# Kernel tuning notes

Hardware: AMD Instinct MI355X
Metric: run time of the kernel (lower is better)

## Reference

```python
import jax, jax.numpy as jnp
import numpy as np
import math

# Static problem sizes (match input_specs)
B, TQ, SQ, TK, SK = 1, 8, 256, 32, 1024
DM, NH = 1024, 8
HD = DM // NH            # 128; mrope_section sums to HD//2
MROPE = [16, 24, 24]
ROPE_BASE = 10000.0


def _build_indices():
    """Reproduce create_idx_cube + slow/fast index selection (all static)."""
    T_max = max(TQ, TK)
    H_max = int(math.sqrt(max(SQ, SK)))
    cube = np.stack(np.meshgrid(np.arange(T_max), np.arange(H_max), np.arange(H_max), indexing='ij'), axis=-1)  # (T,H,W,3)
    # slow (query) indices
    t_idx = np.linspace(0, T_max - 1, TQ).astype(int)
    slow = cube[t_idx]
    if SQ < SK:
        h_q = int(math.sqrt(SQ))
        hi = np.linspace(0, H_max, 2 * h_q + 1).astype(int)[1:-1][::2]
        slow = slow[:, hi][:, :, hi]
    # fast (key) indices
    h_k = int(math.sqrt(SK))
    hf = np.linspace(0, H_max, 2 * h_k + 1).astype(int)[1:-1][::2]
    fast = cube[:, hf][:, :, hf]
    return slow.reshape(-1, 3).T, fast.reshape(-1, 3).T, max(T_max, H_max)


_slow_np, _fast_np, _SEQ = _build_indices()
SLOW_POS = jnp.asarray(_slow_np)   # (3, TQ*SQ) int
FAST_POS = jnp.asarray(_fast_np)   # (3, TK*SK) int

# Standard rotary tables: cos/sin of shape (seq_len, HD)
_inv = 1.0 / (ROPE_BASE ** (np.arange(0, HD, 2, dtype=np.float32) / HD))
_freqs = np.outer(np.arange(_SEQ, dtype=np.float32), _inv)
_emb = np.concatenate([_freqs, _freqs], axis=-1)
COS = jnp.asarray(np.cos(_emb), dtype=jnp.float32)
SIN = jnp.asarray(np.sin(_emb), dtype=jnp.float32)

# per-channel axis (t/h/w) selector, equivalent to the split/concat with i%3
AXIS_MAP = jnp.asarray(np.concatenate([np.full(m, i % 3) for i, m in enumerate(MROPE * 2)]))  # (HD,)


def rotate_half(x):
    return jnp.concatenate([-x[..., HD // 2:], x[..., :HD // 2]], axis=-1)


def apply_mrope(x, pos):
    # x: (B, NH, N, HD); pos: (3, N)
    cos_g = jnp.take_along_axis(COS[pos], AXIS_MAP[None, None, :], axis=0)[0]  # (N, HD)
    sin_g = jnp.take_along_axis(SIN[pos], AXIS_MAP[None, None, :], axis=0)[0]
    return x * cos_g[None, None] + rotate_half(x) * sin_g[None, None]


def setup_inputs() -> dict:
    key = jax.random.key(0)
    ks = jax.random.split(key, 9)
    s = 0.02
    return {
        'q': jax.random.normal(ks[0], (B, TQ, SQ, DM), jnp.float32),
        'k': jax.random.normal(ks[1], (B, TK, SK, DM), jnp.float32),
        'v': jax.random.normal(ks[2], (B, TK, SK, DM), jnp.float32),
        'Wq': jax.random.normal(ks[3], (DM, DM), jnp.float32) * s,
        'bq': jnp.zeros((DM,), jnp.float32),
        'Wk': jax.random.normal(ks[4], (DM, DM), jnp.float32) * s,
        'bk': jnp.zeros((DM,), jnp.float32),
        'Wv': jax.random.normal(ks[5], (DM, DM), jnp.float32) * s,
        'bv': jnp.zeros((DM,), jnp.float32),
    }


def reference(q, k, v, Wq, bq, Wk, bk, Wv, bv):
    # QKV projections -> (B, NH, N, HD)
    qh = (q.reshape(B, TQ * SQ, DM) @ Wq + bq).reshape(B, TQ * SQ, NH, HD).transpose(0, 2, 1, 3)
    kh = (k.reshape(B, TK * SK, DM) @ Wk + bk).reshape(B, TK * SK, NH, HD).transpose(0, 2, 1, 3)
    vh = (v.reshape(B, TK * SK, DM) @ Wv + bv).reshape(B, TK * SK, NH, HD).transpose(0, 2, 1, 3)
    # multimodal 3D RoPE on q (slow frames) and k (fast frames)
    qh = apply_mrope(qh, SLOW_POS)
    kh = apply_mrope(kh, FAST_POS)
    # group time: each query frame attends to its r = TK//TQ aligned kv frames
    r = TK // TQ
    qg = qh.reshape(NH, TQ, SQ, HD).transpose(1, 0, 2, 3)          # (TQ, NH, SQ, HD)
    kg = kh.reshape(NH, TQ, r * SK, HD).transpose(1, 0, 2, 3)      # (TQ, NH, r*SK, HD)
    vg = vh.reshape(NH, TQ, r * SK, HD).transpose(1, 0, 2, 3)
    scores = jnp.einsum('thqd,thkd->thqk', qg, kg) / math.sqrt(HD)
    attn = jax.nn.softmax(scores, axis=-1)
    out = jnp.einsum('thqk,thkd->thqd', attn, vg)                  # (TQ, NH, SQ, HD)
    return out.transpose(0, 2, 1, 3).reshape(B, TQ, SQ, DM)
```

## Files before the change

### kernel.cpp

```cpp
#include <hip/hip_runtime.h>

typedef __bf16 bf16;
typedef __bf16 bf16x8 __attribute__((ext_vector_type(8)));
typedef float  f32x4  __attribute__((ext_vector_type(4)));

#define MFMA16(a, b, c) __builtin_amdgcn_mfma_f32_16x16x32_bf16((a), (b), (c), 0, 0, 0)

#define GLOAD_LDS16(gptr, lptr)                                              \
    __builtin_amdgcn_global_load_lds(                                        \
        (const __attribute__((address_space(1))) unsigned int*)(gptr),       \
        (__attribute__((address_space(3))) unsigned int*)(lptr), 16, 0, 0)

constexpr int kDM = 1024;
constexpr int kNTOK = 32768;

static __device__ inline f32x4 zero4() { f32x4 z = {0.f, 0.f, 0.f, 0.f}; return z; }

__global__ __launch_bounds__(256) void transpose_all(
    const float* __restrict__ Wq, const float* __restrict__ Wk,
    const float* __restrict__ Wv, bf16* __restrict__ Wqt,
    bf16* __restrict__ Wkt, bf16* __restrict__ Wvt)
{
    __shared__ bf16 T[64][68];
    const float* W = (blockIdx.z == 0) ? Wq : (blockIdx.z == 1) ? Wk : Wv;
    bf16* Wt       = (blockIdx.z == 0) ? Wqt : (blockIdx.z == 1) ? Wkt : Wvt;
    const int tid = threadIdx.x;
    const int n0 = blockIdx.x * 64, k0 = blockIdx.y * 64;
    #pragma unroll
    for (int i = 0; i < 4; i++) {
        const int kk = (tid >> 4) + i * 16, nn4 = (tid & 15) * 4;
        float4 v = *(const float4*)&W[(size_t)(k0 + kk) * kDM + n0 + nn4];
        T[nn4 + 0][kk] = (bf16)v.x; T[nn4 + 1][kk] = (bf16)v.y;
        T[nn4 + 2][kk] = (bf16)v.z; T[nn4 + 3][kk] = (bf16)v.w;
    }
    __syncthreads();
    #pragma unroll
    for (int i = 0; i < 4; i++) {
        const int nn = (tid >> 4) + i * 16, kc = (tid & 15) * 4;
        *(ushort4*)&Wt[(size_t)(n0 + nn) * kDM + k0 + kc] = *(const ushort4*)&T[nn][kc];
    }
}

__global__ __launch_bounds__(512, 2) void gemm_fused_all(
    const float* __restrict__ Xq, const float* __restrict__ Xk,
    const float* __restrict__ Xv, const bf16* __restrict__ Wqt,
    const bf16* __restrict__ Wkt, const bf16* __restrict__ Wvt,
    const float* __restrict__ bq, const float* __restrict__ bk,
    const float* __restrict__ bv, bf16* __restrict__ qh,
    bf16* __restrict__ kh, bf16* __restrict__ vt)
{
    __shared__ char smem[163840];

    int b = blockIdx.x;
    const float* X; const bf16* Wt; const float* bias; bf16* out;
    int mtiles, mode;
    if (b < 512)       { X = Xk; Wt = Wkt; bias = bk; out = kh; mtiles = 16; mode = 2; }
    else if (b < 1024) { b -= 512; X = Xv; Wt = Wvt; bias = bv; out = vt; mtiles = 16; mode = 3; }
    else               { b -= 1024; X = Xq; Wt = Wqt; bias = bq; out = qh; mtiles = 1; mode = 1; }

    const int xcd  = b & 7;
    const int s    = b >> 3;
    const int m0   = (xcd * mtiles + (s >> 2)) * 256;
    const int n0   = (s & 3) * 256;
    const int tid  = threadIdx.x;
    const int wave = tid >> 6;
    const int lane = tid & 63;
    const int quad = lane >> 4, l16 = lane & 15;
    const int wr   = wave >> 2;
    const int wc   = wave & 3;

    const int arow  = tid >> 3;
    const int as8   = tid & 7;
    const int awoff = (as8 ^ (arow & 7)) * 8;
    const float* xbase = X + (size_t)(m0 + arow) * kDM + as8 * 8;
    const int bc0 = wave * 4;

    f32x4 acc[8][4];
    #pragma unroll
    for (int i = 0; i < 8; i++)
        #pragma unroll
        for (int j = 0; j < 4; j++) acc[i][j] = zero4();

    auto stageB = [&](int kk, char* dst) {
        #pragma unroll
        for (int i = 0; i < 4; i++) {
            const int row = (bc0 + i) * 8 + (lane >> 3);
            GLOAD_LDS16(&Wt[(size_t)(n0 + row) * kDM + kk + (((lane & 7) ^ (row & 7)) * 8)],
                        (bf16*)dst + (bc0 + i) * 512);
        }
    };
    auto computeKs = [&](const bf16* Ac, const bf16* Bc, int ks) {
        bf16x8 a[8], bfr[4];
        const int G = ks * 4 + quad;
        #pragma unroll
        for (int i = 0; i < 8; i++)
            a[i] = *(const bf16x8*)&Ac[(wr * 128 + i * 16 + l16) * 64 + ((G ^ (l16 & 7)) * 8)];
        #pragma unroll
        for (int j = 0; j < 4; j++)
            bfr[j] = *(const bf16x8*)&Bc[(wc * 64 + j * 16 + l16) * 64 + ((G ^ (l16 & 7)) * 8)];
        #pragma unroll
        for (int i = 0; i < 8; i++)
            #pragma unroll
            for (int j = 0; j < 4; j++)
                acc[i][j] = MFMA16(a[i], bfr[j], acc[i][j]);
    };

    {
        stageB(0, smem + 65536);
        __builtin_amdgcn_sched_barrier(0);
        float4 av[8];
        #pragma unroll
        for (int p = 0; p < 4; p++) {
            const float* src = xbase + (size_t)p * 64 * kDM;
            av[p * 2]     = *(const float4*)src;
            av[p * 2 + 1] = *(const float4*)(src + 4);
        }
        __builtin_amdgcn_sched_barrier(0);
        stageB(64, smem + 98304);
        __builtin_amdgcn_sched_barrier(0);
        asm volatile("s_waitcnt vmcnt(4)" ::: "memory");
        bf16* A0 = (bf16*)smem;
        #pragma unroll
        for (int p = 0; p < 4; p++) {
            bf16x8 w;
            #pragma unroll
            for (int e = 0; e < 4; e++) {
                w[e]     = (bf16)av[p * 2][e];
                w[4 + e] = (bf16)av[p * 2 + 1][e];
            }
            *(bf16x8*)&A0[(p * 64 + arow) * 64 + awoff] = w;
        }
        asm volatile("s_waitcnt lgkmcnt(0)" ::: "memory");
        __builtin_amdgcn_sched_barrier(0);
        __builtin_amdgcn_s_barrier();
    }

    int c3 = 0, p3 = 2;
    for (int t = 0; t < 16; ++t) {
        const bf16* Ac = (const bf16*)(smem + (t & 1) * 32768);
        bf16*       An = (bf16*)(smem + ((t + 1) & 1) * 32768);
        const bf16* Bc = (const bf16*)(smem + 65536 + c3 * 32768);
        char*       Bp = smem + 65536 + p3 * 32768;

        float4 av[8];
        if (t < 15) {
            const int k1 = (t + 1) * 64;
            #pragma unroll
            for (int p = 0; p < 4; p++) {
                const float* src = xbase + (size_t)p * 64 * kDM + k1;
                av[p * 2]     = *(const float4*)src;
                av[p * 2 + 1] = *(const float4*)(src + 4);
            }
        }
        __builtin_amdgcn_sched_barrier(0);
        if (t < 14) stageB((t + 2) * 64, Bp);
        __builtin_amdgcn_sched_barrier(0);

        computeKs(Ac, Bc, 0);

        if (t < 15) {
            #pragma unroll
            for (int p = 0; p < 4; p++) {
                bf16x8 w;
                #pragma unroll
                for (int e = 0; e < 4; e++) {
                    w[e]     = (bf16)av[p * 2][e];
                    w[4 + e] = (bf16)av[p * 2 + 1][e];
                }
                *(bf16x8*)&An[(p * 64 + arow) * 64 + awoff] = w;
            }
        }

        computeKs(Ac, Bc, 1);

        if (t < 14) asm volatile("s_waitcnt vmcnt(4)" ::: "memory");
        else        asm volatile("s_waitcnt vmcnt(0)" ::: "memory");
        asm volatile("s_waitcnt lgkmcnt(0)" ::: "memory");
        __builtin_amdgcn_sched_barrier(0);
        __builtin_amdgcn_s_barrier();
        c3 = (c3 == 2) ? 0 : c3 + 1;
        p3 = (p3 == 2) ? 0 : p3 + 1;
    }

    if (mode == 3) {
        bf16* Y3 = (bf16*)smem;
        #pragma unroll
        for (int h = 0; h < 2; h++) {
            if ((wc >> 1) == h) {
                #pragma unroll
                for (int j = 0; j < 4; j++) {
                    const int nl = (wc & 1) * 64 + j * 16 + l16;
                    const float bv = bias[n0 + wc * 64 + j * 16 + l16];
                    #pragma unroll
                    for (int i = 0; i < 8; i++) {
                        bf16 tmp[4];
                        #pragma unroll
                        for (int r = 0; r < 4; r++) tmp[r] = (bf16)(acc[i][j][r] + bv);
                        *(ushort4*)&Y3[nl * 264 + wr * 128 + i * 16 + quad * 4] =
                            *(const ushort4*)tmp;
                    }
                }
            }
            __syncthreads();
            const int nl = tid >> 5, m8 = (tid & 31) * 8;
            #pragma unroll
            for (int kk = 0; kk < 8; kk++)
                *(uint4*)&out[(size_t)(n0 + h * 128 + nl + kk * 16) * kNTOK + m0 + m8] =
                    *(const uint4*)&Y3[(nl + kk * 16) * 264 + m8];
            __syncthreads();
        }
    } else {
        bf16* Y = (bf16*)smem;
        #pragma unroll
        for (int h = 0; h < 2; h++) {
            if ((wc >> 1) == h && (wc & 1)) {
                #pragma unroll
                for (int j = 0; j < 4; j++) {
                    const int dj = j * 16 + l16;
                    const float bv = bias[n0 + wc * 64 + j * 16 + l16];
                    #pragma unroll
                    for (int i = 0; i < 8; i++)
                        #pragma unroll
                        for (int r = 0; r < 4; r++)
                            Y[(wr * 128 + i * 16 + quad * 4 + r) * 136 + 64 + dj] =
                                (bf16)(acc[i][j][r] + bv);
                }
            }
            __syncthreads();
            if ((wc >> 1) == h && !(wc & 1)) {
                #pragma unroll
                for (int j = 0; j < 4; j++) {
                    const int d = j * 16 + l16;
                    const float bv = bias[n0 + wc * 64 + j * 16 + l16];
                    const float invf = exp2f((float)d * -0.20762050593045951f);
                    #pragma unroll
                    for (int i = 0; i < 8; i++) {
                        #pragma unroll
                        for (int r = 0; r < 4; r++) {
                            const int mloc = wr * 128 + i * 16 + quad * 4 + r;
                            const int tok = m0 + mloc;
                            int pt, ph, pw;
                            if (mode == 2) { pt = tok >> 10; ph = (tok >> 5) & 31; pw = tok & 31; }
                            else { int tq = tok >> 8; pt = (31 * tq) / 7;
                                   ph = 2 * ((tok >> 4) & 15) + 1; pw = 2 * (tok & 15) + 1; }
                            const int p = (d < 16) ? pt : ((d < 40) ? ph : pw);
                            float sn, cs;
                            __sincosf((float)p * invf, &sn, &cs);
                            const float x1 = acc[i][j][r] + bv;
                            const float x2 = (float)Y[mloc * 136 + 64 + d];
                            Y[mloc * 136 + d]      = (bf16)(x1 * cs - x2 * sn);
                            Y[mloc * 136 + 64 + d] = (bf16)(x2 * cs + x1 * sn);
                        }
                    }
                }
            }
            __syncthreads();
            const int rrow = tid >> 1, seg = (tid & 1) * 64;
            #pragma unroll
            for (int kk = 0; kk < 8; kk++)
                *(uint4*)&out[(size_t)(m0 + rrow) * kDM + n0 + h * 128 + seg + kk * 8] =
                    *(const uint4*)&Y[rrow * 136 + seg + kk * 8];
            __syncthreads();
        }
    }
}

__global__ __launch_bounds__(256) void attn_kernel(
    const bf16* __restrict__ qh, const bf16* __restrict__ kh,
    const bf16* __restrict__ vt, float* __restrict__ Opart, float* __restrict__ ml)
{
    __shared__ bf16 Ks[64 * 128];
    __shared__ bf16 Vs[128 * 64];
    __shared__ bf16 Ps[4][16][64];

    const int tid  = threadIdx.x;
    const int z    = blockIdx.x, h = blockIdx.y, qb = blockIdx.z;
    const int t    = z >> 2, sp = z & 3;
    const int wave = tid >> 6;
    const int lane = tid & 63;
    const int quad = lane >> 4, l16 = lane & 15;

    const int qrow = qb * 64 + wave * 16 + l16;
    const size_t qbase = ((size_t)(t * 256 + qrow)) * kDM + h * 128;
    bf16x8 aq[4];
    #pragma unroll
    for (int kb = 0; kb < 4; kb++)
        aq[kb] = *(const bf16x8*)&qh[qbase + kb * 32 + quad * 8];

    bf16x8 ones;
    #pragma unroll
    for (int e = 0; e < 8; e++) ones[e] = (bf16)1.0f;

    f32x4 o[9];
    #pragma unroll
    for (int j = 0; j < 9; j++) o[j] = zero4();
    float m_run[4];
    #pragma unroll
    for (int r = 0; r < 4; r++) m_run[r] = -1e30f;
    const float scale = 0.08838834764831845f;

    const int r16 = lane >> 4, j16 = lane & 15;
    const int r8  = lane >> 3, j8  = lane & 7;

    for (int kt = 0; kt < 16; kt++) {
        const int kbase = t * 4096 + sp * 1024 + kt * 64;
        __syncthreads();
        #pragma unroll
        for (int i = 0; i < 4; i++) {
            const int c = wave * 4 + i;
            const int krow = c * 4 + r16;
            GLOAD_LDS16(&kh[(size_t)(kbase + krow) * kDM + h * 128 + ((j16 ^ (krow & 15)) * 8)],
                        &Ks[c * 512]);
        }
        #pragma unroll
        for (int i = 0; i < 4; i++) {
            const int c = wave * 4 + i;
            GLOAD_LDS16(&vt[(size_t)(h * 128 + c * 8 + r8) * kNTOK + kbase + ((j8 ^ r8) * 8)],
                        &Vs[c * 512]);
        }
        __syncthreads();

        f32x4 s[4];
        #pragma unroll
        for (int c = 0; c < 4; c++) s[c] = zero4();
        __builtin_amdgcn_s_setprio(1);
        #pragma unroll
        for (int kb = 0; kb < 4; kb++) {
            #pragma unroll
            for (int c = 0; c < 4; c++) {
                bf16x8 b = *(const bf16x8*)&Ks[(c * 16 + l16) * 128 + (((kb * 4 + quad) ^ l16) * 8)];
                s[c] = MFMA16(aq[kb], b, s[c]);
            }
        }
        __builtin_amdgcn_s_setprio(0);

        float alpha[4];
        #pragma unroll
        for (int r = 0; r < 4; r++) {
            float sv[4];
            #pragma unroll
            for (int c = 0; c < 4; c++) sv[c] = s[c][r] * scale;
            float mx = fmaxf(fmaxf(sv[0], sv[1]), fmaxf(sv[2], sv[3]));
            #pragma unroll
            for (int off = 1; off < 16; off <<= 1) mx = fmaxf(mx, __shfl_xor(mx, off));
            const float mn = fmaxf(m_run[r], mx);
            alpha[r] = __expf(m_run[r] - mn);
            m_run[r] = mn;
            const int q7 = quad * 4 + r;
            #pragma unroll
            for (int c = 0; c < 4; c++) {
                const int col = (c * 16 + l16) ^ ((q7 & 7) * 8);
                Ps[wave][q7][col] = (bf16)__expf(sv[c] - mn);
            }
        }
        #pragma unroll
        for (int j = 0; j < 9; j++)
            #pragma unroll
            for (int r = 0; r < 4; r++) o[j][r] *= alpha[r];
        __builtin_amdgcn_s_setprio(1);
        #pragma unroll
        for (int ks = 0; ks < 2; ks++) {
            bf16x8 pa = *(const bf16x8*)&Ps[wave][l16][((ks * 4 + quad) ^ (l16 & 7)) * 8];
            #pragma unroll
            for (int j = 0; j < 8; j++) {
                bf16x8 bv = *(const bf16x8*)&Vs[(j * 16 + l16) * 64 + (((ks * 4 + quad) ^ (l16 & 7)) * 8)];
                o[j] = MFMA16(pa, bv, o[j]);
            }
            o[8] = MFMA16(pa, ones, o[8]);
        }
        __builtin_amdgcn_s_setprio(0);
    }

    #pragma unroll
    for (int r = 0; r < 4; r++) {
        const int srow = qb * 64 + wave * 16 + quad * 4 + r;
        const size_t pr = ((size_t)(z * 8 + h)) * 256 + srow;
        #pragma unroll
        for (int j = 0; j < 8; j++)
            Opart[pr * 128 + j * 16 + l16] = o[j][r];
        if (l16 == 0) { ml[pr * 2] = m_run[r]; ml[pr * 2 + 1] = o[8][r]; }
    }
}

__global__ __launch_bounds__(256) void combine_kernel(
    const float* __restrict__ Opart, const float* __restrict__ ml,
    float* __restrict__ out)
{
    const int tid = threadIdx.x;
    const int rid = blockIdx.x * 2 + (tid >> 7);
    const int d   = tid & 127;
    const int t = rid >> 11, h = (rid >> 8) & 7, srow = rid & 255;

    float mv[4], lv[4];
    #pragma unroll
    for (int sp = 0; sp < 4; sp++) {
        const size_t pr = ((size_t)((t * 4 + sp) * 8 + h)) * 256 + srow;
        float2 p = *(const float2*)&ml[pr * 2];
        mv[sp] = p.x; lv[sp] = p.y;
    }
    const float ms = fmaxf(fmaxf(mv[0], mv[1]), fmaxf(mv[2], mv[3]));
    float lsum = 0.f, acc = 0.f;
    #pragma unroll
    for (int sp = 0; sp < 4; sp++) {
        const size_t pr = ((size_t)((t * 4 + sp) * 8 + h)) * 256 + srow;
        const float w = __expf(mv[sp] - ms);
        lsum += lv[sp] * w;
        acc  += Opart[pr * 128 + d] * w;
    }
    out[((size_t)(t * 256 + srow)) * kDM + h * 128 + d] = acc / lsum;
}

extern "C" void kernel_launch(void* const* d_in, const int* in_sizes, int n_in,
                              void* d_out, int out_size, void* d_ws, size_t ws_size,
                              hipStream_t stream)
{
    const float* q  = (const float*)d_in[0];
    const float* k  = (const float*)d_in[1];
    const float* v  = (const float*)d_in[2];
    const float* Wq = (const float*)d_in[3];
    const float* bq = (const float*)d_in[4];
    const float* Wk = (const float*)d_in[5];
    const float* bk = (const float*)d_in[6];
    const float* Wv = (const float*)d_in[7];
    const float* bv = (const float*)d_in[8];
    float* out = (float*)d_out;

    bf16* qh  = (bf16*)d_ws;
    bf16* kh  = qh + (size_t)2048 * 1024;
    bf16* vt  = kh + (size_t)32768 * 1024;
    bf16* Wqt = vt + (size_t)32768 * 1024;
    bf16* Wkt = Wqt + (size_t)1024 * 1024;
    bf16* Wvt = Wkt + (size_t)1024 * 1024;
    float* Opart = (float*)(Wvt + (size_t)1024 * 1024);
    float* ml    = Opart + (size_t)32 * 8 * 256 * 128;

    transpose_all<<<dim3(16, 16, 3), 256, 0, stream>>>(Wq, Wk, Wv, Wqt, Wkt, Wvt);
    gemm_fused_all<<<1056, 512, 0, stream>>>(q, k, v, Wqt, Wkt, Wvt,
                                             bq, bk, bv, qh, kh, vt);
    attn_kernel<<<dim3(32, 8, 4), 256, 0, stream>>>(qh, kh, vt, Opart, ml);
    combine_kernel<<<8192, 256, 0, stream>>>(Opart, ml, out);
}
```

Measured before the change: 659.5 us.

## Pre-convert activations to bf16 and restructure projection GEMM with quadrant pipelining

Result: faster. 634.4 us (-3.8%).

```diff
diff --git a/kernel.cpp b/kernel.cpp
--- a/kernel.cpp
+++ b/kernel.cpp
@@ -15,6 +15,39 @@
 constexpr int kNTOK = 32768;
 
 static __device__ inline f32x4 zero4() { f32x4 z = {0.f, 0.f, 0.f, 0.f}; return z; }
+
+__global__ __launch_bounds__(256) void cvt_qk(
+    const float* __restrict__ q, const float* __restrict__ k, bf16* __restrict__ dst)
+{
+    const int q8 = 262144, tot = q8 + 4194304;
+    int idx = blockIdx.x * 256 + threadIdx.x;
+    const int stride = gridDim.x * 256;
+    for (; idx < tot; idx += stride) {
+        const float* s = (idx < q8) ? q + (size_t)idx * 8
+                                    : k + (size_t)(idx - q8) * 8;
+        const float4 u0 = *(const float4*)s;
+        const float4 u1 = *(const float4*)(s + 4);
+        bf16x8 w;
+        w[0] = (bf16)u0.x; w[1] = (bf16)u0.y; w[2] = (bf16)u0.z; w[3] = (bf16)u0.w;
+        w[4] = (bf16)u1.x; w[5] = (bf16)u1.y; w[6] = (bf16)u1.z; w[7] = (bf16)u1.w;
+        *(bf16x8*)&dst[(size_t)idx * 8] = w;
+    }
+}
+
+__global__ __launch_bounds__(256) void cvt_bf16(
+    const float* __restrict__ src, bf16* __restrict__ dst, int n8)
+{
+    int idx = blockIdx.x * 256 + threadIdx.x;
+    const int stride = gridDim.x * 256;
+    for (; idx < n8; idx += stride) {
+        const float4 u0 = *(const float4*)(src + (size_t)idx * 8);
+        const float4 u1 = *(const float4*)(src + (size_t)idx * 8 + 4);
+        bf16x8 w;
+        w[0] = (bf16)u0.x; w[1] = (bf16)u0.y; w[2] = (bf16)u0.z; w[3] = (bf16)u0.w;
+        w[4] = (bf16)u1.x; w[5] = (bf16)u1.y; w[6] = (bf16)u1.z; w[7] = (bf16)u1.w;
+        *(bf16x8*)&dst[(size_t)idx * 8] = w;
+    }
+}
 
 __global__ __launch_bounds__(256) void transpose_all(
     const float* __restrict__ Wq, const float* __restrict__ Wk,
@@ -41,39 +74,47 @@
     }
 }
 
-__global__ __launch_bounds__(512, 2) void gemm_fused_all(
-    const float* __restrict__ Xq, const float* __restrict__ Xk,
-    const float* __restrict__ Xv, const bf16* __restrict__ Wqt,
-    const bf16* __restrict__ Wkt, const bf16* __restrict__ Wvt,
-    const float* __restrict__ bq, const float* __restrict__ bk,
-    const float* __restrict__ bv, bf16* __restrict__ qh,
-    bf16* __restrict__ kh, bf16* __restrict__ vt)
-{
-    __shared__ char smem[163840];
-
-    int b = blockIdx.x;
-    const float* X; const bf16* Wt; const float* bias; bf16* out;
-    int mtiles, mode;
-    if (b < 512)       { X = Xk; Wt = Wkt; bias = bk; out = kh; mtiles = 16; mode = 2; }
-    else if (b < 1024) { b -= 512; X = Xv; Wt = Wvt; bias = bv; out = vt; mtiles = 16; mode = 3; }
-    else               { b -= 1024; X = Xq; Wt = Wqt; bias = bq; out = qh; mtiles = 1; mode = 1; }
-
-    const int xcd  = b & 7;
-    const int s    = b >> 3;
-    const int m0   = (xcd * mtiles + (s >> 2)) * 256;
-    const int n0   = (s & 3) * 256;
+__device__ __forceinline__ void gemm256_body(
+    const bf16* __restrict__ X, const bf16* __restrict__ Wt,
+    const float* __restrict__ bias, bf16* __restrict__ out,
+    int m0, int n0, int mode)
+{
+    __shared__ char smem[131072];
+    bf16* SA = (bf16*)smem;
+    bf16* SB = (bf16*)(smem + 65536);
+
     const int tid  = threadIdx.x;
     const int wave = tid >> 6;
     const int lane = tid & 63;
     const int quad = lane >> 4, l16 = lane & 15;
     const int wr   = wave >> 2;
     const int wc   = wave & 3;
-
-    const int arow  = tid >> 3;
-    const int as8   = tid & 7;
-    const int awoff = (as8 ^ (arow & 7)) * 8;
-    const float* xbase = X + (size_t)(m0 + arow) * kDM + as8 * 8;
-    const int bc0 = wave * 4;
+    const int r8   = lane >> 3, j8 = lane & 7;
+    const int c0   = wave * 2;
+
+    const bf16* aS00 = X  + (size_t)(m0 +   0 + c0 * 8 + r8) * kDM + (j8 ^ r8) * 8;
+    const bf16* aS01 = X  + (size_t)(m0 +   8 + c0 * 8 + r8) * kDM + (j8 ^ r8) * 8;
+    const bf16* aS10 = X  + (size_t)(m0 + 128 + c0 * 8 + r8) * kDM + (j8 ^ r8) * 8;
+    const bf16* aS11 = X  + (size_t)(m0 + 136 + c0 * 8 + r8) * kDM + (j8 ^ r8) * 8;
+    const bf16* bS00 = Wt + (size_t)(n0 +   0 + c0 * 8 + r8) * kDM + (j8 ^ r8) * 8;
+    const bf16* bS01 = Wt + (size_t)(n0 +   8 + c0 * 8 + r8) * kDM + (j8 ^ r8) * 8;
+    const bf16* bS10 = Wt + (size_t)(n0 + 128 + c0 * 8 + r8) * kDM + (j8 ^ r8) * 8;
+    const bf16* bS11 = Wt + (size_t)(n0 + 136 + c0 * 8 + r8) * kDM + (j8 ^ r8) * 8;
+
+    auto stageA = [&](int T, int h) {
+        bf16* dst = SA + (T & 1) * 16384 + h * 8192 + c0 * 512;
+        if (h == 0) { GLOAD_LDS16(aS00 + (size_t)T * 64, dst);
+                      GLOAD_LDS16(aS01 + (size_t)T * 64, dst + 512); }
+        else        { GLOAD_LDS16(aS10 + (size_t)T * 64, dst);
+                      GLOAD_LDS16(aS11 + (size_t)T * 64, dst + 512); }
+    };
+    auto stageB = [&](int T, int h) {
+        bf16* dst = SB + (T & 1) * 16384 + h * 8192 + c0 * 512;
+        if (h == 0) { GLOAD_LDS16(bS00 + (size_t)T * 64, dst);
+                      GLOAD_LDS16(bS01 + (size_t)T * 64, dst + 512); }
+        else        { GLOAD_LDS16(bS10 + (size_t)T * 64, dst);
+                      GLOAD_LDS16(bS11 + (size_t)T * 64, dst + 512); }
+    };
 
     f32x4 acc[8][4];
     #pragma unroll
@@ -81,105 +122,83 @@
         #pragma unroll
         for (int j = 0; j < 4; j++) acc[i][j] = zero4();
 
-    auto stageB = [&](int kk, char* dst) {
-        #pragma unroll
-        for (int i = 0; i < 4; i++) {
-            const int row = (bc0 + i) * 8 + (lane >> 3);
-            GLOAD_LDS16(&Wt[(size_t)(n0 + row) * kDM + kk + (((lane & 7) ^ (row & 7)) * 8)],
-                        (bf16*)dst + (bc0 + i) * 512);
-        }
-    };
-    auto computeKs = [&](const bf16* Ac, const bf16* Bc, int ks) {
-        bf16x8 a[8], bfr[4];
-        const int G = ks * 4 + quad;
-        #pragma unroll
-        for (int i = 0; i < 8; i++)
-            a[i] = *(const bf16x8*)&Ac[(wr * 128 + i * 16 + l16) * 64 + ((G ^ (l16 & 7)) * 8)];
-        #pragma unroll
-        for (int j = 0; j < 4; j++)
-            bfr[j] = *(const bf16x8*)&Bc[(wc * 64 + j * 16 + l16) * 64 + ((G ^ (l16 & 7)) * 8)];
-        #pragma unroll
-        for (int i = 0; i < 8; i++)
-            #pragma unroll
-            for (int j = 0; j < 4; j++)
-                acc[i][j] = MFMA16(a[i], bfr[j], acc[i][j]);
-    };
-
-    {
-        stageB(0, smem + 65536);
-        __builtin_amdgcn_sched_barrier(0);
-        float4 av[8];
-        #pragma unroll
-        for (int p = 0; p < 4; p++) {
-            const float* src = xbase + (size_t)p * 64 * kDM;
-            av[p * 2]     = *(const float4*)src;
-            av[p * 2 + 1] = *(const float4*)(src + 4);
-        }
-        __builtin_amdgcn_sched_barrier(0);
-        stageB(64, smem + 98304);
-        __builtin_amdgcn_sched_barrier(0);
-        asm volatile("s_waitcnt vmcnt(4)" ::: "memory");
-        bf16* A0 = (bf16*)smem;
-        #pragma unroll
-        for (int p = 0; p < 4; p++) {
-            bf16x8 w;
-            #pragma unroll
-            for (int e = 0; e < 4; e++) {
-                w[e]     = (bf16)av[p * 2][e];
-                w[4 + e] = (bf16)av[p * 2 + 1][e];
-            }
-            *(bf16x8*)&A0[(p * 64 + arow) * 64 + awoff] = w;
-        }
-        asm volatile("s_waitcnt lgkmcnt(0)" ::: "memory");
-        __builtin_amdgcn_sched_barrier(0);
-        __builtin_amdgcn_s_barrier();
-    }
-
-    int c3 = 0, p3 = 2;
-    for (int t = 0; t < 16; ++t) {
-        const bf16* Ac = (const bf16*)(smem + (t & 1) * 32768);
-        bf16*       An = (bf16*)(smem + ((t + 1) & 1) * 32768);
-        const bf16* Bc = (const bf16*)(smem + 65536 + c3 * 32768);
-        char*       Bp = smem + 65536 + p3 * 32768;
-
-        float4 av[8];
-        if (t < 15) {
-            const int k1 = (t + 1) * 64;
-            #pragma unroll
-            for (int p = 0; p < 4; p++) {
-                const float* src = xbase + (size_t)p * 64 * kDM + k1;
-                av[p * 2]     = *(const float4*)src;
-                av[p * 2 + 1] = *(const float4*)(src + 4);
-            }
-        }
-        __builtin_amdgcn_sched_barrier(0);
-        if (t < 14) stageB((t + 2) * 64, Bp);
-        __builtin_amdgcn_sched_barrier(0);
-
-        computeKs(Ac, Bc, 0);
-
-        if (t < 15) {
-            #pragma unroll
-            for (int p = 0; p < 4; p++) {
-                bf16x8 w;
-                #pragma unroll
-                for (int e = 0; e < 4; e++) {
-                    w[e]     = (bf16)av[p * 2][e];
-                    w[4 + e] = (bf16)av[p * 2 + 1][e];
-                }
-                *(bf16x8*)&An[(p * 64 + arow) * 64 + awoff] = w;
-            }
-        }
-
-        computeKs(Ac, Bc, 1);
-
-        if (t < 14) asm volatile("s_waitcnt vmcnt(4)" ::: "memory");
-        else        asm volatile("s_waitcnt vmcnt(0)" ::: "memory");
-        asm volatile("s_waitcnt lgkmcnt(0)" ::: "memory");
-        __builtin_amdgcn_sched_barrier(0);
-        __builtin_amdgcn_s_barrier();
-        c3 = (c3 == 2) ? 0 : c3 + 1;
-        p3 = (p3 == 2) ? 0 : p3 + 1;
+    stageA(0, 0); stageA(0, 1); stageB(0, 0); stageB(0, 1);
+    stageA(1, 0); stageA(1, 1);
+    asm volatile("s_waitcnt vmcnt(4)" ::: "memory");
+    __builtin_amdgcn_s_barrier();
+    __builtin_amdgcn_sched_barrier(0);
+
+    bf16x8 af[4][2], bf[2][2];
+
+    for (int w = 0; w < 16; ++w) {
+        const int d = w & 1;
+        const bf16* Acur = SA + d * 16384 + wr * 8192;
+        const bf16* Bcur = SB + d * 16384 + (wc >> 1) * 8192;
+
+        auto loadAF = [&](int IH) {
+            #pragma unroll
+            for (int i2 = 0; i2 < 4; i2++)
+                #pragma unroll
+                for (int ks = 0; ks < 2; ks++)
+                    af[i2][ks] = *(const bf16x8*)&Acur[
+                        (IH * 64 + i2 * 16 + l16) * 64 + (((ks * 4 + quad) ^ (l16 & 7)) * 8)];
+        };
+        auto loadBF = [&](int JH) {
+            #pragma unroll
+            for (int j2 = 0; j2 < 2; j2++)
+                #pragma unroll
+                for (int ks = 0; ks < 2; ks++)
+                    bf[j2][ks] = *(const bf16x8*)&Bcur[
+                        ((wc & 1) * 64 + JH * 32 + j2 * 16 + l16) * 64 +
+                        (((ks * 4 + quad) ^ (l16 & 7)) * 8)];
+        };
+        auto mfmaQ = [&](int IB, int JB) {
+            __builtin_amdgcn_s_setprio(1);
+            #pragma unroll
+            for (int ks = 0; ks < 2; ks++)
+                #pragma unroll
+                for (int i2 = 0; i2 < 4; i2++)
+                    #pragma unroll
+                    for (int j2 = 0; j2 < 2; j2++)
+                        acc[IB + i2][JB + j2] =
+                            MFMA16(af[i2][ks], bf[j2][ks], acc[IB + i2][JB + j2]);
+            __builtin_amdgcn_s_setprio(0);
+        };
+
+        loadAF(0); loadBF(0);
+        if (w < 15) stageB(w + 1, 0);
+        __builtin_amdgcn_sched_barrier(0);
+        __builtin_amdgcn_s_barrier();
+        __builtin_amdgcn_sched_barrier(0);
+        mfmaQ(0, 0);
+        __builtin_amdgcn_s_barrier();
+        __builtin_amdgcn_sched_barrier(0);
+        loadBF(1);
+        if (w < 15) stageB(w + 1, 1);
+        __builtin_amdgcn_sched_barrier(0);
+        __builtin_amdgcn_s_barrier();
+        __builtin_amdgcn_sched_barrier(0);
+        mfmaQ(0, 2);
+        __builtin_amdgcn_s_barrier();
+        __builtin_amdgcn_sched_barrier(0);
+        loadAF(1);
+        __builtin_amdgcn_sched_barrier(0);
+        __builtin_amdgcn_s_barrier();
+        __builtin_amdgcn_sched_barrier(0);
+        mfmaQ(4, 2);
+        __builtin_amdgcn_s_barrier();
+        __builtin_amdgcn_sched_barrier(0);
+        loadBF(0);
+        if (w < 14) { stageA(w + 2, 0); stageA(w + 2, 1); }
+        __builtin_amdgcn_sched_barrier(0);
+        __builtin_amdgcn_s_barrier();
+        __builtin_amdgcn_sched_barrier(0);
+        mfmaQ(4, 0);
+        if (w < 14)       asm volatile("s_waitcnt vmcnt(4)" ::: "memory");
+        else if (w == 14) asm volatile("s_waitcnt vmcnt(0)" ::: "memory");
+        __builtin_amdgcn_sched_barrier(0);
+        __builtin_amdgcn_s_barrier();
+        __builtin_amdgcn_sched_barrier(0);
     }
 
     if (mode == 3) {
@@ -230,9 +249,9 @@
             if ((wc >> 1) == h && !(wc & 1)) {
                 #pragma unroll
                 for (int j = 0; j < 4; j++) {
-                    const int d = j * 16 + l16;
+                    const int d2 = j * 16 + l16;
                     const float bv = bias[n0 + wc * 64 + j * 16 + l16];
-                    const float invf = exp2f((float)d * -0.20762050593045951f);
+                    const float invf = exp2f((float)d2 * -0.20762050593045951f);
                     #pragma unroll
                     for (int i = 0; i < 8; i++) {
                         #pragma unroll
@@ -243,13 +262,13 @@
                             if (mode == 2) { pt = tok >> 10; ph = (tok >> 5) & 31; pw = tok & 31; }
                             else { int tq = tok >> 8; pt = (31 * tq) / 7;
                                    ph = 2 * ((tok >> 4) & 15) + 1; pw = 2 * (tok & 15) + 1; }
-                            const int p = (d < 16) ? pt : ((d < 40) ? ph : pw);
+                            const int p = (d2 < 16) ? pt : ((d2 < 40) ? ph : pw);
                             float sn, cs;
                             __sincosf((float)p * invf, &sn, &cs);
                             const float x1 = acc[i][j][r] + bv;
-                            const float x2 = (float)Y[mloc * 136 + 64 + d];
-                            Y[mloc * 136 + d]      = (bf16)(x1 * cs - x2 * sn);
-                            Y[mloc * 136 + 64 + d] = (bf16)(x2 * cs + x1 * sn);
+                            const float x2 = (float)Y[mloc * 136 + 64 + d2];
+                            Y[mloc * 136 + d2]      = (bf16)(x1 * cs - x2 * sn);
+                            Y[mloc * 136 + 64 + d2] = (bf16)(x2 * cs + x1 * sn);
                         }
                     }
                 }
@@ -263,6 +282,32 @@
             __syncthreads();
         }
     }
+}
+
+__global__ __launch_bounds__(512, 2) void gemm256_kq(
+    const bf16* __restrict__ Xk, const bf16* __restrict__ Xq,
+    const bf16* __restrict__ Wkt, const bf16* __restrict__ Wqt,
+    const float* __restrict__ bk, const float* __restrict__ bq,
+    bf16* __restrict__ kh, bf16* __restrict__ qh)
+{
+    int b = blockIdx.x;
+    if (b < 512) {
+        const int xcd = b & 7, s = b >> 3;
+        gemm256_body(Xk, Wkt, bk, kh, (xcd * 16 + (s >> 2)) * 256, (s & 3) * 256, 2);
+    } else {
+        b -= 512;
+        const int xcd = b & 7, s = b >> 3;
+        gemm256_body(Xq, Wqt, bq, qh, xcd * 256, (s & 3) * 256, 1);
+    }
+}
+
+__global__ __launch_bounds__(512, 2) void gemm256_v(
+    const bf16* __restrict__ Xv, const bf16* __restrict__ Wvt,
+    const float* __restrict__ bv, bf16* __restrict__ vt)
+{
+    const int b = blockIdx.x;
+    const int xcd = b & 7, s = b >> 3;
+    gemm256_body(Xv, Wvt, bv, vt, (xcd * 16 + (s >> 2)) * 256, (s & 3) * 256, 3);
 }
 
 __global__ __launch_bounds__(256) void attn_kernel(
@@ -433,10 +478,18 @@
     bf16* Wvt = Wkt + (size_t)1024 * 1024;
     float* Opart = (float*)(Wvt + (size_t)1024 * 1024);
     float* ml    = Opart + (size_t)32 * 8 * 256 * 128;
+    bf16* Xb     = (bf16*)(ml + (size_t)32 * 8 * 256 * 2);
+    bf16* Xq     = Xb;
+    bf16* Xk     = Xb + (size_t)2048 * 1024;
 
     transpose_all<<<dim3(16, 16, 3), 256, 0, stream>>>(Wq, Wk, Wv, Wqt, Wkt, Wvt);
-    gemm_fused_all<<<1056, 512, 0, stream>>>(q, k, v, Wqt, Wkt, Wvt,
-                                             bq, bk, bv, qh, kh, vt);
+
+    cvt_qk<<<2048, 256, 0, stream>>>(q, k, Xb);
+    gemm256_kq<<<544, 512, 0, stream>>>(Xk, Xq, Wkt, Wqt, bk, bq, kh, qh);
+
+    cvt_bf16<<<2048, 256, 0, stream>>>(v, Xb, 32768 * 1024 / 8);
+    gemm256_v<<<512, 512, 0, stream>>>(Xb, Wvt, bv, vt);
+
     attn_kernel<<<dim3(32, 8, 4), 256, 0, stream>>>(qh, kh, vt, Opart, ml);
     combine_kernel<<<8192, 256, 0, stream>>>(Opart, ml, out);
 }
```
